# Kernel tuning notes

Measured on AMD Instinct MI355X. Metric: run time of the kernel, lower is better.

The kernel has to match this reference:

```python
import jax, jax.numpy as jnp
import numpy as np

NUM_NODES = 100000
NUM_EDGES = 1600000
NUM_GRAPHS = 64
IN_DIM = 128
HID = 128
OUT_DIM = 256
NUM_LAYERS = 5
BN_EPS = 1e-5


def _bn(t, gamma, beta):
    # BatchNorm1d forward with batch statistics (biased variance), as in train mode
    m = jnp.mean(t, axis=0)
    v = jnp.var(t, axis=0)
    return gamma * (t - m) * jax.lax.rsqrt(v + BN_EPS) + beta


def setup_inputs() -> dict:
    key = jax.random.key(0)
    ks = jax.random.split(key, 16)
    x = jax.random.normal(ks[0], (NUM_NODES, IN_DIM), dtype=jnp.float32)
    edge_index = jax.random.randint(ks[1], (2, NUM_EDGES), 0, NUM_NODES, dtype=jnp.int64)
    batch = jnp.sort(jax.random.randint(ks[2], (NUM_NODES,), 0, NUM_GRAPHS, dtype=jnp.int64))
    s1 = 1.0 / np.sqrt(IN_DIM)
    s2 = 1.0 / np.sqrt(HID)
    # stacked per-layer GIN MLP params: Linear(HID,HID) -> BN -> ReLU -> Linear(HID,HID)
    w1 = jax.random.normal(ks[3], (NUM_LAYERS, HID, HID), dtype=jnp.float32) * s1
    b1 = jnp.zeros((NUM_LAYERS, HID), dtype=jnp.float32)
    gamma1 = jnp.ones((NUM_LAYERS, HID), dtype=jnp.float32)
    beta1 = jnp.zeros((NUM_LAYERS, HID), dtype=jnp.float32)
    w2 = jax.random.normal(ks[4], (NUM_LAYERS, HID, HID), dtype=jnp.float32) * s2
    b2 = jnp.zeros((NUM_LAYERS, HID), dtype=jnp.float32)
    # outer per-layer BatchNorm after each GINConv
    gamma_bn = jnp.ones((NUM_LAYERS, HID), dtype=jnp.float32)
    beta_bn = jnp.zeros((NUM_LAYERS, HID), dtype=jnp.float32)
    # output projection Linear(HID, OUT_DIM)
    wp = jax.random.normal(ks[5], (HID, OUT_DIM), dtype=jnp.float32) * s2
    bp = jnp.zeros((OUT_DIM,), dtype=jnp.float32)
    return {"x": x, "edge_index": edge_index, "batch": batch,
            "w1": w1, "b1": b1, "gamma1": gamma1, "beta1": beta1,
            "w2": w2, "b2": b2, "gamma_bn": gamma_bn, "beta_bn": beta_bn,
            "wp": wp, "bp": bp}


def reference(x, edge_index, batch, w1, b1, gamma1, beta1, w2, b2, gamma_bn, beta_bn, wp, bp):
    src, dst = edge_index[0], edge_index[1]
    h = x
    for i in range(NUM_LAYERS):
        # GINConv, eps=0: mlp((1+eps)*h + sum_{j in N(i)} h_j)
        agg = jax.ops.segment_sum(h[src], dst, num_segments=NUM_NODES)
        z = h + agg
        t = _bn(z @ w1[i] + b1[i], gamma1[i], beta1[i])
        t = jax.nn.relu(t)
        t = t @ w2[i] + b2[i]
        # outer BatchNorm + ReLU (dropout p handled as identity in eval)
        t = jax.nn.relu(_bn(t, gamma_bn[i], beta_bn[i]))
        h = h + t  # residual (dims always match)
    node_emb = h
    # global mean pool per graph
    sums = jax.ops.segment_sum(h, batch, num_segments=NUM_GRAPHS)
    counts = jax.ops.segment_sum(jnp.ones((NUM_NODES,), dtype=h.dtype), batch, num_segments=NUM_GRAPHS)
    pooled = sums / jnp.maximum(counts, 1.0)[:, None]
    graph_emb = pooled @ wp + bp
    return graph_emb, node_emb
```

## Files before the change

kernel.cpp:

```cpp
#include <hip/hip_runtime.h>

#define NNODES 100000
#define NEDGES 1600000
#define NGRAPHS 64
#define HID 128
#define OUTD 256
#define NLAYERS 5
#define BN_EPS 1e-5f
#define NBUCK 196
#define BUCKCAP 9216
#define FILL_BLOCKS 391
#define NREP1 64
#define NREP2 8
#define AG1B 6250

typedef __attribute__((ext_vector_type(8))) short short8;
typedef __attribute__((ext_vector_type(4))) float f32x4;

__device__ inline unsigned short f2b(float f) {
    union { float f; unsigned int u; } a; a.f = f;
    unsigned int u = a.u;
    return (unsigned short)((u + 0x7FFF + ((u >> 16) & 1)) >> 16);
}
__device__ inline float b2f(unsigned short b) {
    union { unsigned int u; float f; } a; a.u = ((unsigned int)b) << 16;
    return a.f;
}

union U8 { short8 v; unsigned short u[8]; };

__global__ void k_init(const float* __restrict__ x, float* __restrict__ h,
                       ushort* __restrict__ hb,
                       const float* __restrict__ w1, const float* __restrict__ w2,
                       unsigned short* __restrict__ WT, int* __restrict__ bcur) {
    int b = blockIdx.x;
    if (b < 12500) {
        int i = b * 256 + threadIdx.x;
        float4 v = ((const float4*)x)[i];
        ((float4*)h)[i] = v;
        ushort4 o;
        o.x = f2b(v.x); o.y = f2b(v.y); o.z = f2b(v.z); o.w = f2b(v.w);
        ((ushort4*)hb)[i] = o;
    } else {
        int t = (b - 12500) * 256 + threadIdx.x;
        int mat = t >> 14;
        int rem = t & 16383;
        int k = rem >> 7, n = rem & 127;
        const float* src = (mat < 5) ? &w1[(size_t)mat * 16384]
                                     : &w2[(size_t)(mat - 5) * 16384];
        WT[(size_t)mat * 16384 + n * 128 + k] = f2b(src[k * 128 + n]);
        if (b == 12500 && threadIdx.x < NBUCK)
            bcur[threadIdx.x] = threadIdx.x * BUCKCAP;
    }
}

__global__ __launch_bounds__(256) void k_fill1(
    const int* __restrict__ srcv, const int* __restrict__ dstv,
    int* __restrict__ bcur, unsigned int* __restrict__ packed) {
    __shared__ int hist[NBUCK];
    __shared__ int base[NBUCK];
    int tid = threadIdx.x;
    int e0 = blockIdx.x * 4096;
    for (int i = tid; i < NBUCK; i += 256) hist[i] = 0;
    __syncthreads();
#pragma unroll
    for (int i = 0; i < 16; i++) {
        int e = e0 + i * 256 + tid;
        if (e < NEDGES) atomicAdd(&hist[dstv[e] >> 9], 1);
    }
    __syncthreads();
    for (int i = tid; i < NBUCK; i += 256) {
        int c = hist[i];
        base[i] = c ? atomicAdd(&bcur[i], c) : 0;
        hist[i] = 0;
    }
    __syncthreads();
#pragma unroll
    for (int i = 0; i < 16; i++) {
        int e = e0 + i * 256 + tid;
        if (e < NEDGES) {
            int d = dstv[e];
            int b = d >> 9;
            int r = atomicAdd(&hist[b], 1);
            packed[base[b] + r] = ((unsigned int)srcv[e] << 9) | (unsigned int)(d & 511);
        }
    }
}

__global__ __launch_bounds__(256) void k_fill2(
    const unsigned int* __restrict__ packed, const int* __restrict__ bcur,
    int2* __restrict__ off2, int* __restrict__ adj, int* __restrict__ dhist) {
    __shared__ int deg[512];
    __shared__ int cur[512];
    __shared__ int dh[64];
    int tid = threadIdx.x;
    int b = blockIdx.x;
    int base = b * BUCKCAP;
    int cnt = bcur[b] - base;
    deg[tid] = 0; deg[tid + 256] = 0;
    if (tid < 64) dh[tid] = 0;
    __syncthreads();
    for (int i = tid; i < cnt; i += 256)
        atomicAdd(&deg[packed[base + i] & 511], 1);
    __syncthreads();
    cur[tid] = deg[tid]; cur[tid + 256] = deg[tid + 256];
    __syncthreads();
    for (int o = 1; o < 512; o <<= 1) {
        int u0 = (tid >= o) ? cur[tid - o] : 0;
        int u1 = (tid + 256 >= o) ? cur[tid + 256 - o] : 0;
        __syncthreads();
        cur[tid] += u0; cur[tid + 256] += u1;
        __syncthreads();
    }
    int nbase = b * 512;
#pragma unroll
    for (int i = 0; i < 2; i++) {
        int t = tid + i * 256;
        int st = base + cur[t] - deg[t];
        int n = nbase + t;
        if (n < NNODES) {
            off2[n] = make_int2(st, st + deg[t]);
            int d = deg[t]; if (d > 63) d = 63;
            atomicAdd(&dh[d], 1);
        }
    }
    __syncthreads();
    if (tid < 64 && dh[tid]) atomicAdd(&dhist[tid * 16], dh[tid]);
#pragma unroll
    for (int i = 0; i < 2; i++) {
        int t = tid + i * 256;
        cur[t] = base + cur[t] - deg[t];
    }
    __syncthreads();
    for (int i = tid; i < cnt; i += 256) {
        unsigned int p = packed[base + i];
        int r = atomicAdd(&cur[p & 511], 1);
        adj[r] = (int)(p >> 9);
    }
}

__global__ void k_dscan(const int* __restrict__ dhist, int* __restrict__ dcur) {
    if (threadIdx.x == 0) {
        int s = 0;
        for (int i = 63; i >= 0; i--) { int c = dhist[i * 16]; dcur[i * 16] = s; s += c; }
    }
}

__global__ __launch_bounds__(256) void k_dscat(
    const int2* __restrict__ off2, int* __restrict__ dcur,
    int* __restrict__ perm, int2* __restrict__ off2p) {
    __shared__ int h[64], base[64];
    int tid = threadIdx.x;
    int n = blockIdx.x * 256 + tid;
    if (tid < 64) h[tid] = 0;
    __syncthreads();
    int d = 0; int2 oo = make_int2(0, 0);
    if (n < NNODES) {
        oo = off2[n];
        d = oo.y - oo.x; if (d > 63) d = 63;
        atomicAdd(&h[d], 1);
    }
    __syncthreads();
    if (tid < 64) { int c = h[tid]; base[tid] = c ? atomicAdd(&dcur[tid * 16], c) : 0; h[tid] = 0; }
    __syncthreads();
    if (n < NNODES) {
        int r = atomicAdd(&h[d], 1);
        int pos = base[d] + r;
        perm[pos] = n;
        off2p[pos] = oo;
    }
}

__global__ __launch_bounds__(256) void k_ag1(
    const ushort* __restrict__ hb, const int2* __restrict__ off2p,
    const int* __restrict__ adj, const int* __restrict__ perm,
    const unsigned short* __restrict__ WT,
    const float* __restrict__ bias, ushort* __restrict__ C,
    float* __restrict__ stats) {
    __shared__ ushort zt[16 * 128];
    __shared__ float lstat[256];
    int tid = threadIdx.x;
    int n = tid >> 4;
    int c = tid & 15;
    int idx = blockIdx.x * 16 + n;
    int node = perm[idx];
    int2 oo = off2p[idx];
    const short8* hb8 = (const short8*)hb;

    U8 sv; sv.v = hb8[(size_t)node * 16 + c];
    float acc[8];
#pragma unroll
    for (int k = 0; k < 8; k++) acc[k] = b2f(sv.u[k]);

    int e = oo.x, e1 = oo.y;
    for (; e + 8 <= e1; e += 8) {
        int s[8];
#pragma unroll
        for (int j = 0; j < 8; j++) s[j] = adj[e + j];
        U8 u[8];
#pragma unroll
        for (int j = 0; j < 8; j++) u[j].v = hb8[(size_t)s[j] * 16 + c];
#pragma unroll
        for (int j = 0; j < 8; j++)
#pragma unroll
            for (int k = 0; k < 8; k++) acc[k] += b2f(u[j].u[k]);
    }
    for (; e + 4 <= e1; e += 4) {
        int s0 = adj[e], s1 = adj[e + 1], s2 = adj[e + 2], s3 = adj[e + 3];
        U8 u0, u1, u2, u3;
        u0.v = hb8[(size_t)s0 * 16 + c];
        u1.v = hb8[(size_t)s1 * 16 + c];
        u2.v = hb8[(size_t)s2 * 16 + c];
        u3.v = hb8[(size_t)s3 * 16 + c];
#pragma unroll
        for (int k = 0; k < 8; k++)
            acc[k] += (b2f(u0.u[k]) + b2f(u1.u[k])) + (b2f(u2.u[k]) + b2f(u3.u[k]));
    }
    for (; e < e1; e++) {
        int s = adj[e];
        U8 u; u.v = hb8[(size_t)s * 16 + c];
#pragma unroll
        for (int k = 0; k < 8; k++) acc[k] += b2f(u.u[k]);
    }

    U8 o;
#pragma unroll
    for (int k = 0; k < 8; k++) o.u[k] = f2b(acc[k]);
    *(short8*)((char*)zt + ((n * 256 + c * 16) ^ ((n & 7) << 4))) = o.v;
    __syncthreads();

    int wave = tid >> 6;
    int lane = tid & 63;
    int q = lane >> 4;
    int l16 = lane & 15;

    f32x4 gacc[2];
    gacc[0] = (f32x4){0.f, 0.f, 0.f, 0.f};
    gacc[1] = (f32x4){0.f, 0.f, 0.f, 0.f};

#pragma unroll
    for (int kc = 0; kc < 4; kc++) {
        int k0 = kc * 32 + q * 8;
        int ch = kc * 4 + q;
        short8 av = *(const short8*)(
            (char*)zt + ((l16 * 256 + ch * 16) ^ ((l16 & 7) << 4)));
#pragma unroll
        for (int nt = 0; nt < 2; nt++) {
            int col0 = (wave * 2 + nt) * 16;
            short8 bf = *(const short8*)&WT[(size_t)(col0 + l16) * 128 + k0];
            gacc[nt] = __builtin_amdgcn_mfma_f32_16x16x32_bf16(
                av, bf, gacc[nt], 0, 0, 0);
        }
    }

    int rowbase = blockIdx.x * 16;
    int prow[4];
#pragma unroll
    for (int r = 0; r < 4; r++) prow[r] = perm[rowbase + q * 4 + r];
#pragma unroll
    for (int nt = 0; nt < 2; nt++) {
        int col = (wave * 2 + nt) * 16 + l16;
        float b = bias[col];
        float csum = 0.f, csq = 0.f;
#pragma unroll
        for (int r = 0; r < 4; r++) {
            float v = gacc[nt][r] + b;
            C[(size_t)prow[r] * 128 + col] = f2b(v);
            csum += v; csq += v * v;
        }
        csum += __shfl_xor(csum, 16, 64); csq += __shfl_xor(csq, 16, 64);
        csum += __shfl_xor(csum, 32, 64); csq += __shfl_xor(csq, 32, 64);
        if (q == 0) { lstat[col] = csum; lstat[128 + col] = csq; }
    }
    __syncthreads();
    atomicAdd(&stats[((blockIdx.x & (NREP1 - 1)) << 8) + tid], lstat[tid]);
}

__global__ __launch_bounds__(256) void k_gemm2(
    const ushort* __restrict__ A, const unsigned short* __restrict__ WT,
    const float* __restrict__ bias, ushort* __restrict__ C,
    const float* __restrict__ statsIn, const float* __restrict__ gamma,
    const float* __restrict__ beta, float* __restrict__ stats) {
    __shared__ ushort wlds[16384];
    __shared__ float lstat[256];
    __shared__ float s_sc[128], s_sh[128];
    int tid = threadIdx.x;

#pragma unroll
    for (int it = 0; it < 8; it++) {
        int i = tid * 8 + it * 2048;
        int row = i >> 7;
        short8 v = *(const short8*)&WT[i];
        *(short8*)((char*)wlds + ((i * 2) ^ ((row & 7) << 4))) = v;
    }

    if (tid < 128) {
        float s = 0.f, qq = 0.f;
#pragma unroll
        for (int r = 0; r < NREP1; r++) {
            s  += statsIn[r * 256 + tid];
            qq += statsIn[r * 256 + 128 + tid];
        }
        float m = s * (1.f / NNODES);
        float var = qq * (1.f / NNODES) - m * m;
        float sc = gamma[tid] * rsqrtf(var + BN_EPS);
        s_sc[tid] = sc;
        s_sh[tid] = beta[tid] - m * sc;
    }
    lstat[tid] = 0.f;

    int wave = tid >> 6;
    int lane = tid & 63;
    int q = lane >> 4;
    int l16 = lane & 15;
    int rowbase = blockIdx.x * 128 + wave * 32;

    short8 araw[2][4];
#pragma unroll
    for (int rt = 0; rt < 2; rt++) {
        int row = rowbase + rt * 16 + l16;
        if (row >= NNODES) row = NNODES - 1;
#pragma unroll
        for (int kc = 0; kc < 4; kc++)
            araw[rt][kc] = *(const short8*)&A[(size_t)row * 128 + kc * 32 + q * 8];
    }

    f32x4 acc[2][8];
#pragma unroll
    for (int rt = 0; rt < 2; rt++)
#pragma unroll
        for (int nt = 0; nt < 8; nt++) acc[rt][nt] = (f32x4){0.f, 0.f, 0.f, 0.f};

    __syncthreads();

#pragma unroll
    for (int kc = 0; kc < 4; kc++) {
        int k0 = kc * 32 + q * 8;
        short8 bf[8];
#pragma unroll
        for (int nt = 0; nt < 8; nt++) {
            int row = nt * 16 + l16;
            bf[nt] = *(const short8*)(
                (char*)wlds + ((row * 256 + k0 * 2) ^ ((row & 7) << 4)));
        }

        float4 s0 = *(const float4*)&s_sc[k0];
        float4 s1 = *(const float4*)&s_sc[k0 + 4];
        float4 t0 = *(const float4*)&s_sh[k0];
        float4 t1 = *(const float4*)&s_sh[k0 + 4];
        float scl[8] = {s0.x, s0.y, s0.z, s0.w, s1.x, s1.y, s1.z, s1.w};
        float shf[8] = {t0.x, t0.y, t0.z, t0.w, t1.x, t1.y, t1.z, t1.w};
#pragma unroll
        for (int rt = 0; rt < 2; rt++) {
            union { short8 s; unsigned short u[8]; } in, cv;
            in.s = araw[rt][kc];
#pragma unroll
            for (int j = 0; j < 8; j++) {
                float f = fmaxf(b2f(in.u[j]) * scl[j] + shf[j], 0.f);
                cv.u[j] = f2b(f);
            }
#pragma unroll
            for (int nt = 0; nt < 8; nt++)
                acc[rt][nt] = __builtin_amdgcn_mfma_f32_16x16x32_bf16(
                    cv.s, bf[nt], acc[rt][nt], 0, 0, 0);
        }
    }

#pragma unroll
    for (int nt = 0; nt < 8; nt++) {
        float b = bias[nt * 16 + l16];
        float csum = 0.f, csq = 0.f;
#pragma unroll
        for (int rt = 0; rt < 2; rt++) {
            int rb = rowbase + rt * 16 + q * 4;
#pragma unroll
            for (int r = 0; r < 4; r++) {
                int row = rb + r;
                if (row < NNODES) {
                    float v = acc[rt][nt][r] + b;
                    C[(size_t)row * 128 + nt * 16 + l16] = f2b(v);
                    csum += v; csq += v * v;
                }
            }
        }
        csum += __shfl_xor(csum, 16, 64); csq += __shfl_xor(csq, 16, 64);
        csum += __shfl_xor(csum, 32, 64); csq += __shfl_xor(csq, 32, 64);
        if (q == 0) {
            atomicAdd(&lstat[nt * 16 + l16], csum);
            atomicAdd(&lstat[128 + nt * 16 + l16], csq);
        }
    }
    __syncthreads();
    atomicAdd(&stats[((blockIdx.x & (NREP2 - 1)) << 8) + tid], lstat[tid]);
}

__global__ void k_resid(float* __restrict__ h, ushort* __restrict__ hb,
                        const ushort* __restrict__ t2b,
                        const float* __restrict__ statsIn,
                        const float* __restrict__ gamma, const float* __restrict__ beta) {
    __shared__ float s_sc[128], s_sh[128];
    int tid = threadIdx.x;
    if (tid < 128) {
        float s = 0.f, qq = 0.f;
#pragma unroll
        for (int r = 0; r < NREP2; r++) {
            s  += statsIn[r * 256 + tid];
            qq += statsIn[r * 256 + 128 + tid];
        }
        float m = s * (1.f / NNODES);
        float var = qq * (1.f / NNODES) - m * m;
        float sc = gamma[tid] * rsqrtf(var + BN_EPS);
        s_sc[tid] = sc;
        s_sh[tid] = beta[tid] - m * sc;
    }
    __syncthreads();
    int i = blockIdx.x * 256 + tid;
    int c4 = (i & 31) * 4;
    float4 sc = *(const float4*)&s_sc[c4];
    float4 sh = *(const float4*)&s_sh[c4];
    ushort4 t = ((const ushort4*)t2b)[i];
    float4 hv = ((float4*)h)[i];
    hv.x += fmaxf(b2f(t.x) * sc.x + sh.x, 0.f);
    hv.y += fmaxf(b2f(t.y) * sc.y + sh.y, 0.f);
    hv.z += fmaxf(b2f(t.z) * sc.z + sh.z, 0.f);
    hv.w += fmaxf(b2f(t.w) * sc.w + sh.w, 0.f);
    ((float4*)h)[i] = hv;
    ushort4 o;
    o.x = f2b(hv.x); o.y = f2b(hv.y); o.z = f2b(hv.z); o.w = f2b(hv.w);
    ((ushort4*)hb)[i] = o;
}

__global__ void k_pool(const float* __restrict__ h, const int* __restrict__ batch,
                       float* __restrict__ pooled, float* __restrict__ gcnt) {
    __shared__ float4 red[256];
    __shared__ int lcnt[NGRAPHS];
    int t = threadIdx.x;
    int d4 = t & 31, sub = t >> 5;
    int n0 = blockIdx.x * 128;
    if (n0 >= NNODES) return;
    int n1 = n0 + 128; if (n1 > NNODES) n1 = NNODES;
    if (t < NGRAPHS) lcnt[t] = 0;
    __syncthreads();
    if (t < n1 - n0) atomicAdd(&lcnt[batch[n0 + t]], 1);
    __syncthreads();
    if (t < NGRAPHS && lcnt[t]) atomicAdd(&gcnt[t], (float)lcnt[t]);

    int glo = batch[n0], ghi = batch[n1 - 1];
    for (int g = glo; g <= ghi; g++) {
        float4 acc = make_float4(0.f, 0.f, 0.f, 0.f);
        for (int r = n0 + sub; r < n1; r += 8) {
            if (batch[r] == g) {
                float4 v = ((const float4*)h)[(size_t)r * 32 + d4];
                acc.x += v.x; acc.y += v.y; acc.z += v.z; acc.w += v.w;
            }
        }
        red[t] = acc;
        __syncthreads();
        if (sub < 4) {
            float4 o = red[t + 128];
            red[t].x += o.x; red[t].y += o.y; red[t].z += o.z; red[t].w += o.w;
        }
        __syncthreads();
        if (sub < 2) {
            float4 o = red[t + 64];
            red[t].x += o.x; red[t].y += o.y; red[t].z += o.z; red[t].w += o.w;
        }
        __syncthreads();
        if (sub == 0) {
            float4 o = red[t + 32];
            float4 a = red[t];
            a.x += o.x; a.y += o.y; a.z += o.z; a.w += o.w;
            atomicAdd(&pooled[g * 128 + d4 * 4 + 0], a.x);
            atomicAdd(&pooled[g * 128 + d4 * 4 + 1], a.y);
            atomicAdd(&pooled[g * 128 + d4 * 4 + 2], a.z);
            atomicAdd(&pooled[g * 128 + d4 * 4 + 3], a.w);
        }
        __syncthreads();
    }
}

__global__ void k_proj(const float* __restrict__ pooled, const float* __restrict__ cnt,
                       const float* __restrict__ wp, const float* __restrict__ bp,
                       float* __restrict__ out) {
    __shared__ float prow[128];
    int g = blockIdx.x, c = threadIdx.x;
    if (c < 128) prow[c] = pooled[g * 128 + c] / fmaxf(cnt[g], 1.f);
    __syncthreads();
    float acc = bp[c];
    for (int k = 0; k < 128; k++) acc += prow[k] * wp[k * 256 + c];
    out[g * 256 + c] = acc;
}

extern "C" void kernel_launch(void* const* d_in, const int* in_sizes, int n_in,
                              void* d_out, int out_size, void* d_ws, size_t ws_size,
                              hipStream_t stream) {
    const float* x    = (const float*)d_in[0];
    const int*   eidx = (const int*)d_in[1];
    const int*   batch= (const int*)d_in[2];
    const float* w1   = (const float*)d_in[3];
    const float* b1   = (const float*)d_in[4];
    const float* g1   = (const float*)d_in[5];
    const float* be1  = (const float*)d_in[6];
    const float* w2   = (const float*)d_in[7];
    const float* b2   = (const float*)d_in[8];
    const float* gbn  = (const float*)d_in[9];
    const float* bbn  = (const float*)d_in[10];
    const float* wp   = (const float*)d_in[11];
    const float* bp   = (const float*)d_in[12];

    float* out  = (float*)d_out;
    float* gemb = out;
    float* h    = out + (size_t)NGRAPHS * OUTD;

    char* w = (char*)d_ws;
    ushort* hb   = (ushort*)w; w += (size_t)NNODES * 128 * 2;
    ushort* t2b  = (ushort*)w; w += (size_t)NNODES * 128 * 2;
    ushort* tb   = (ushort*)w; w += (size_t)NNODES * 128 * 2;
    int2*  off2  = (int2*)w;  w += (size_t)NNODES * 8;
    int*   adj   = (int*)w;   w += (size_t)NBUCK * BUCKCAP * 4;
    unsigned short* WT = (unsigned short*)w; w += (size_t)10 * 16384 * 2;
    int*   bcur  = (int*)w;   w += 256 * 4;
    float* statsAll = (float*)w; w += (size_t)NLAYERS * (NREP1 + NREP2) * 256 * 4;
    float* pooled= (float*)w; w += (size_t)NGRAPHS * HID * 4;
    float* gcnt  = (float*)w; w += NGRAPHS * 4;
    int*   dhist = (int*)w;   w += 1024 * 4;
    int*   dcur  = (int*)w;   w += 1024 * 4;
    int*   perm  = (int*)w;   w += (size_t)NNODES * 4;
    int2*  off2p = (int2*)w;  w += (size_t)NNODES * 8;

    unsigned int* packed = (unsigned int*)tb;

    const int* srcv = eidx;
    const int* dstv = eidx + NEDGES;

    k_init<<<12500 + 640, 256, 0, stream>>>(x, h, hb, w1, w2, WT, bcur);

    hipMemsetAsync(statsAll, 0,
                   ((size_t)NLAYERS * (NREP1 + NREP2) * 256 + NGRAPHS * HID + NGRAPHS
                    + 2048) * 4, stream);

    k_fill1<<<FILL_BLOCKS, 256, 0, stream>>>(srcv, dstv, bcur, packed);
    k_fill2<<<NBUCK, 256, 0, stream>>>(packed, bcur, off2, adj, dhist);
    k_dscan<<<1, 64, 0, stream>>>(dhist, dcur);
    k_dscat<<<(NNODES + 255) / 256, 256, 0, stream>>>(off2, dcur, perm, off2p);

    for (int i = 0; i < NLAYERS; i++) {
        float* st1 = statsAll + (size_t)i * (NREP1 + NREP2) * 256;
        float* st2 = st1 + (size_t)NREP1 * 256;
        k_ag1<<<AG1B, 256, 0, stream>>>(
            hb, off2p, adj, perm, WT + (size_t)i * 16384, b1 + i * HID, tb, st1);
        k_gemm2<<<(NNODES + 127) / 128, 256, 0, stream>>>(
            tb, WT + (size_t)(5 + i) * 16384, b2 + i * HID, t2b,
            st1, g1 + i * HID, be1 + i * HID, st2);
        k_resid<<<NNODES * 128 / 4 / 256, 256, 0, stream>>>(
            h, hb, t2b, st2, gbn + i * HID, bbn + i * HID);
    }

    k_pool<<<(NNODES + 127) / 128, 256, 0, stream>>>(h, batch, pooled, gcnt);
    k_proj<<<NGRAPHS, 256, 0, stream>>>(pooled, gcnt, wp, bp, gemb);
}
```

Before: 889.5 us.

## Halve gemm2 rows per block, double stat replicas, reverse degree-sort order

The second GEMM kernel now gives each wave 16 rows instead of 32 and each block 64 rows instead of 128, so it launches about twice as many blocks. This raises parallelism and occupancy but loads the weight tile into LDS and reduces block statistics twice as often. The number of replicated stat accumulators doubles to spread atomic contention across the extra blocks. The degree-bucket scan now runs in ascending rather than descending order, which changes the node permutation used by the aggregation kernel and so the order in which nodes are scheduled.

```diff
diff --git a/kernel.cpp b/kernel.cpp
--- a/kernel.cpp
+++ b/kernel.cpp
@@ -11,8 +11,9 @@
 #define BUCKCAP 9216
 #define FILL_BLOCKS 391
 #define NREP1 64
-#define NREP2 8
+#define NREP2 16
 #define AG1B 6250
+#define G2B 1563
 
 typedef __attribute__((ext_vector_type(8))) short short8;
 typedef __attribute__((ext_vector_type(4))) float f32x4;
@@ -142,7 +143,7 @@
 __global__ void k_dscan(const int* __restrict__ dhist, int* __restrict__ dcur) {
     if (threadIdx.x == 0) {
         int s = 0;
-        for (int i = 63; i >= 0; i--) { int c = dhist[i * 16]; dcur[i * 16] = s; s += c; }
+        for (int i = 0; i < 64; i++) { int c = dhist[i * 16]; dcur[i * 16] = s; s += c; }
     }
 }
 
@@ -313,23 +314,18 @@
     int lane = tid & 63;
     int q = lane >> 4;
     int l16 = lane & 15;
-    int rowbase = blockIdx.x * 128 + wave * 32;
-
-    short8 araw[2][4];
-#pragma unroll
-    for (int rt = 0; rt < 2; rt++) {
-        int row = rowbase + rt * 16 + l16;
-        if (row >= NNODES) row = NNODES - 1;
-#pragma unroll
-        for (int kc = 0; kc < 4; kc++)
-            araw[rt][kc] = *(const short8*)&A[(size_t)row * 128 + kc * 32 + q * 8];
-    }
-
-    f32x4 acc[2][8];
-#pragma unroll
-    for (int rt = 0; rt < 2; rt++)
-#pragma unroll
-        for (int nt = 0; nt < 8; nt++) acc[rt][nt] = (f32x4){0.f, 0.f, 0.f, 0.f};
+    int rowbase = blockIdx.x * 64 + wave * 16;
+
+    int arow = rowbase + l16;
+    if (arow >= NNODES) arow = NNODES - 1;
+    short8 araw[4];
+#pragma unroll
+    for (int kc = 0; kc < 4; kc++)
+        araw[kc] = *(const short8*)&A[(size_t)arow * 128 + kc * 32 + q * 8];
+
+    f32x4 acc[8];
+#pragma unroll
+    for (int nt = 0; nt < 8; nt++) acc[nt] = (f32x4){0.f, 0.f, 0.f, 0.f};
 
     __syncthreads();
 
@@ -350,37 +346,31 @@
         float4 t1 = *(const float4*)&s_sh[k0 + 4];
         float scl[8] = {s0.x, s0.y, s0.z, s0.w, s1.x, s1.y, s1.z, s1.w};
         float shf[8] = {t0.x, t0.y, t0.z, t0.w, t1.x, t1.y, t1.z, t1.w};
-#pragma unroll
-        for (int rt = 0; rt < 2; rt++) {
-            union { short8 s; unsigned short u[8]; } in, cv;
-            in.s = araw[rt][kc];
-#pragma unroll
-            for (int j = 0; j < 8; j++) {
-                float f = fmaxf(b2f(in.u[j]) * scl[j] + shf[j], 0.f);
-                cv.u[j] = f2b(f);
-            }
-#pragma unroll
-            for (int nt = 0; nt < 8; nt++)
-                acc[rt][nt] = __builtin_amdgcn_mfma_f32_16x16x32_bf16(
-                    cv.s, bf[nt], acc[rt][nt], 0, 0, 0);
-        }
+        union { short8 s; unsigned short u[8]; } in, cv;
+        in.s = araw[kc];
+#pragma unroll
+        for (int j = 0; j < 8; j++) {
+            float f = fmaxf(b2f(in.u[j]) * scl[j] + shf[j], 0.f);
+            cv.u[j] = f2b(f);
+        }
+#pragma unroll
+        for (int nt = 0; nt < 8; nt++)
+            acc[nt] = __builtin_amdgcn_mfma_f32_16x16x32_bf16(
+                cv.s, bf[nt], acc[nt], 0, 0, 0);
     }
 
 #pragma unroll
     for (int nt = 0; nt < 8; nt++) {
         float b = bias[nt * 16 + l16];
         float csum = 0.f, csq = 0.f;
-#pragma unroll
-        for (int rt = 0; rt < 2; rt++) {
-            int rb = rowbase + rt * 16 + q * 4;
-#pragma unroll
-            for (int r = 0; r < 4; r++) {
-                int row = rb + r;
-                if (row < NNODES) {
-                    float v = acc[rt][nt][r] + b;
-                    C[(size_t)row * 128 + nt * 16 + l16] = f2b(v);
-                    csum += v; csq += v * v;
-                }
+        int rb = rowbase + q * 4;
+#pragma unroll
+        for (int r = 0; r < 4; r++) {
+            int row = rb + r;
+            if (row < NNODES) {
+                float v = acc[nt][r] + b;
+                C[(size_t)row * 128 + nt * 16 + l16] = f2b(v);
+                csum += v; csq += v * v;
             }
         }
         csum += __shfl_xor(csum, 16, 64); csq += __shfl_xor(csq, 16, 64);
@@ -549,7 +539,7 @@
         float* st2 = st1 + (size_t)NREP1 * 256;
         k_ag1<<<AG1B, 256, 0, stream>>>(
             hb, off2p, adj, perm, WT + (size_t)i * 16384, b1 + i * HID, tb, st1);
-        k_gemm2<<<(NNODES + 127) / 128, 256, 0, stream>>>(
+        k_gemm2<<<G2B, 256, 0, stream>>>(
             tb, WT + (size_t)(5 + i) * 16384, b2 + i * HID, t2b,
             st1, g1 + i * HID, be1 + i * HID, st2);
         k_resid<<<NNODES * 128 / 4 / 256, 256, 0, stream>>>(
```

Measured after the change: 858.6 us. 3.5% less time.
